# Performance work log

Hardware: AMD Instinct MI355X
Metric: run time of the kernel (lower is better)

## Reference

```python
import jax, jax.numpy as jnp
import numpy as np

N = 30000
IN_DIM = 256
OUT_DIM = 256
H = 4
HEAD_DIM = OUT_DIM // H  # 64
NUM_EDGE_TYPES = 20
NUM_USED_TYPES = 5  # len(EDGE_TYPES); global indices 0..4
E_PER_TYPE = 40000


def setup_inputs() -> dict:
    key = jax.random.key(0)
    ks = jax.random.split(key, 12)
    s = 0.05
    return {
        "h": jax.random.normal(ks[0], (N, IN_DIM), jnp.float32),
        "edge_src": jax.random.randint(ks[1], (NUM_USED_TYPES, E_PER_TYPE), 0, N, jnp.int64 if jax.config.jax_enable_x64 else jnp.int32),
        "edge_tgt": jax.random.randint(ks[2], (NUM_USED_TYPES, E_PER_TYPE), 0, N, jnp.int64 if jax.config.jax_enable_x64 else jnp.int32),
        "kqv_weight": jax.random.normal(ks[3], (3 * OUT_DIM, IN_DIM), jnp.float32) * s,
        "kqv_bias": jax.random.normal(ks[4], (3 * OUT_DIM,), jnp.float32) * s,
        "out_weight": jax.random.normal(ks[5], (OUT_DIM, OUT_DIM), jnp.float32) * s,
        "out_bias": jax.random.normal(ks[6], (OUT_DIM,), jnp.float32) * s,
        "k_rel": jax.random.normal(ks[7], (NUM_EDGE_TYPES, HEAD_DIM, HEAD_DIM), jnp.float32) * s,
        "v_rel": jax.random.normal(ks[8], (NUM_EDGE_TYPES, HEAD_DIM, HEAD_DIM), jnp.float32) * s,
        "skip": jax.random.normal(ks[9], (1,), jnp.float32),
        "p_rel": jax.random.normal(ks[10], (NUM_USED_TYPES, H), jnp.float32),
    }


def reference(h, edge_src, edge_tgt, kqv_weight, kqv_bias, out_weight, out_bias,
              k_rel, v_rel, skip, p_rel):
    n = h.shape[0]
    T, E = edge_src.shape
    d = HEAD_DIM

    # fused KQV projection: [N, 3*D]
    kqv = h @ kqv_weight.T + kqv_bias
    K, Q, V = jnp.split(kqv, 3, axis=-1)
    K = K.reshape(n, H, d)
    Q = Q.reshape(n, H, d)
    V = V.reshape(n, H, d)

    et = jnp.arange(T)  # global edge-type indices 0..T-1
    k_r = k_rel[et]     # [T, d, d]
    v_r = v_rel[et]

    # gather per-edge, per-type; apply relation matmuls
    K_rel = jnp.einsum('tehd,tdf->tehf', K[edge_src], k_r)  # [T,E,H,d]
    V_rel = jnp.einsum('tehd,tdf->tehf', V[edge_src], v_r)
    Q_tgt = Q[edge_tgt]                                     # [T,E,H,d]

    scale = float(d) ** (-0.5)
    alpha = (Q_tgt * K_rel).sum(-1) * scale                 # [T,E,H]
    alpha = alpha * p_rel[et][:, None, :]                   # multiplicative prior

    # flatten all edge types
    TE = T * E
    alpha = alpha.reshape(TE, H)
    V_rel = V_rel.reshape(TE, H, d)
    tgt_all = edge_tgt.reshape(TE)

    # segmented softmax over incoming edges per target node
    amax = jax.ops.segment_max(alpha, tgt_all, num_segments=n)       # [N,H]
    exp_alpha = jnp.exp(alpha - amax[tgt_all])
    exp_sum = jax.ops.segment_sum(exp_alpha, tgt_all, num_segments=n)
    attn = exp_alpha / (exp_sum[tgt_all] + 1e-16)                    # [TE,H]

    msg = attn[..., None] * V_rel                                    # [TE,H,d]
    out = jax.ops.segment_sum(msg, tgt_all, num_segments=n)          # [N,H,d]
    out = out.reshape(n, OUT_DIM)

    out = jax.nn.gelu(out, approximate=False)
    out = out @ out_weight.T + out_bias

    a = jax.nn.sigmoid(skip)  # [1], broadcasts
    return a * out + (1.0 - a) * h
```

## Files before the change

kernel.cpp:

```cpp
#include <hip/hip_runtime.h>
#include <hip/hip_bf16.h>
#include <math.h>

#define N_NODES 30000
#define NHEAD   4
#define HDIM    64
#define NTYPES  5
#define EPT     40000
#define TE      (NTYPES * EPT)
#define KDIM    256
#define NCAT    1792
#define NBLK    118

typedef __attribute__((ext_vector_type(8))) short short8;
typedef __attribute__((ext_vector_type(4))) float f32x4;

__device__ __forceinline__ unsigned short f2bf(float f) {
    __hip_bfloat16 h = __float2bfloat16(f);
    return *reinterpret_cast<unsigned short*>(&h);
}
__device__ __forceinline__ float bf2f(unsigned short u) {
    return __uint_as_float((unsigned)u << 16);
}

__device__ __forceinline__ void gload16(const unsigned short* g, unsigned short* l) {
    __builtin_amdgcn_global_load_lds((const __attribute__((address_space(1))) void*)g,
                                     (__attribute__((address_space(3))) void*)l, 16, 0, 0);
}

__global__ __launch_bounds__(256) void init_kernel(int* __restrict__ deg) {
    const int gid = blockIdx.x * blockDim.x + threadIdx.x;
    if (gid < N_NODES) deg[gid] = 0;
}

__global__ __launch_bounds__(256) void hist_kernel(const int* __restrict__ etgt,
                                                   int* __restrict__ deg) {
    const int stride = gridDim.x * blockDim.x;
    for (int i = blockIdx.x * blockDim.x + threadIdx.x; i < TE; i += stride)
        atomicAdd(&deg[etgt[i]], 1);
}

__global__ __launch_bounds__(256) void scan1_kernel(const int* __restrict__ deg,
                                                    int* __restrict__ bsum) {
    __shared__ int ws[4];
    const int t = threadIdx.x;
    const int gid = blockIdx.x * 256 + t;
    int d = (gid < N_NODES) ? deg[gid] : 0;
    d += __shfl_xor(d, 1);
    d += __shfl_xor(d, 2);
    d += __shfl_xor(d, 4);
    d += __shfl_xor(d, 8);
    d += __shfl_xor(d, 16);
    d += __shfl_xor(d, 32);
    if ((t & 63) == 0) ws[t >> 6] = d;
    __syncthreads();
    if (t == 0) bsum[blockIdx.x] = ws[0] + ws[1] + ws[2] + ws[3];
}

__global__ __launch_bounds__(128) void scan2_kernel(const int* __restrict__ bsum,
                                                    int* __restrict__ boff) {
    __shared__ int s[128];
    const int t = threadIdx.x;
    s[t] = (t < NBLK) ? bsum[t] : 0;
    __syncthreads();
    for (int d = 1; d < 128; d <<= 1) {
        const int v = (t >= d) ? s[t - d] : 0;
        __syncthreads();
        s[t] += v;
        __syncthreads();
    }
    if (t < NBLK) boff[t] = (t > 0) ? s[t - 1] : 0;
}

__global__ __launch_bounds__(256) void scan3_kernel(const int* __restrict__ deg,
                                                    const int* __restrict__ boff,
                                                    int* __restrict__ off,
                                                    int* __restrict__ cursor) {
    __shared__ int s[256];
    const int t = threadIdx.x;
    const int gid = blockIdx.x * 256 + t;
    const int d = (gid < N_NODES) ? deg[gid] : 0;
    s[t] = d;
    __syncthreads();
    for (int dd = 1; dd < 256; dd <<= 1) {
        const int v = (t >= dd) ? s[t - dd] : 0;
        __syncthreads();
        s[t] += v;
        __syncthreads();
    }
    if (gid < N_NODES) {
        const int excl = s[t] - d + boff[blockIdx.x];
        off[gid] = excl;
        cursor[gid] = excl;
    }
}

__global__ __launch_bounds__(256) void scatter_kernel(const int* __restrict__ etgt,
                                                      const int* __restrict__ esrc,
                                                      int* __restrict__ cursor,
                                                      int* __restrict__ perm) {
    const int stride = gridDim.x * blockDim.x;
    for (int e = blockIdx.x * blockDim.x + threadIdx.x; e < TE; e += stride) {
        const int pos = atomicAdd(&cursor[etgt[e]], 1);
        perm[pos] = esrc[e] | ((e / EPT) << 16);
    }
}

__global__ __launch_bounds__(256) void prep_all(const float* __restrict__ kqv_w,
                                                const float* __restrict__ kqv_b,
                                                const float* __restrict__ k_rel,
                                                const float* __restrict__ p_rel,
                                                const float* __restrict__ h,
                                                const float* __restrict__ v_rel,
                                                const float* __restrict__ out_w,
                                                unsigned short* __restrict__ Wcat,
                                                float* __restrict__ bias_cat,
                                                unsigned short* __restrict__ hb,
                                                unsigned short* __restrict__ vrelT,
                                                unsigned short* __restrict__ Wob) {
    const int bid = blockIdx.x;
    const int tid = threadIdx.x;
    if (bid < 1792) {
        const int r = bid, f = tid;
        if (r < 1280) {
            const int t = r >> 8, hh = (r >> 6) & 3, d = r & 63;
            const float sc = 0.125f * p_rel[t * NHEAD + hh];
            float acc = 0.f;
#pragma unroll
            for (int fp = 0; fp < 64; ++fp)
                acc = fmaf(kqv_w[(size_t)(hh * 64 + fp) * 256 + f], k_rel[t * 4096 + fp * 64 + d], acc);
            Wcat[(size_t)r * 256 + f] = f2bf(acc * sc);
            if (f == 0) {
                float b = 0.f;
#pragma unroll
                for (int fp = 0; fp < 64; ++fp)
                    b = fmaf(kqv_b[hh * 64 + fp], k_rel[t * 4096 + fp * 64 + d], b);
                bias_cat[r] = b * sc;
            }
        } else {
            const int src_row = r - 1024;
            Wcat[(size_t)r * 256 + f] = f2bf(kqv_w[(size_t)src_row * 256 + f]);
            if (f == 0) bias_cat[r] = kqv_b[src_row];
        }
    } else if (bid < 9292) {
        const int i = (bid - 1792) * 256 + tid;
        const float4 v = ((const float4*)h)[i];
        ushort4 u;
        u.x = f2bf(v.x); u.y = f2bf(v.y); u.z = f2bf(v.z); u.w = f2bf(v.w);
        ((ushort4*)hb)[i] = u;
    } else if (bid < 9372) {
        const int idx = (bid - 9292) * 256 + tid;
        if (idx < 64 * 320) {
            const int f = idx / 320, k = idx - f * 320;
            vrelT[f * 320 + k] = f2bf(v_rel[(k >> 6) * 4096 + (k & 63) * 64 + f]);
        }
    } else {
        const int i = (bid - 9372) * 256 + tid;
        Wob[i] = f2bf(out_w[i]);
    }
}

__global__ __launch_bounds__(256) void mfma_gemm(const unsigned short* __restrict__ hb,
                                                 const unsigned short* __restrict__ Wcat,
                                                 const float* __restrict__ bias_cat,
                                                 unsigned short* __restrict__ Ccat) {
    __shared__ unsigned short As[2][128 * 32];
    __shared__ unsigned short Bs[2][128 * 32];
    const int orig = blockIdx.x;
    const int xcd = orig & 7, pos = orig >> 3;
    const int q = 3290 / 8, r = 3290 % 8;
    const int wgid = (xcd < r ? xcd * (q + 1) : r * (q + 1) + (xcd - r) * q) + pos;
    const int brow0 = (wgid / 14) * 128;
    const int bcol0 = (wgid % 14) * 128;

    const int t = threadIdx.x;
    const int wid = t >> 6, lane = t & 63;
    const int wr = wid >> 1, wc = wid & 1;
    const int lrow = lane & 15, kb = lane >> 4;
    const int srow = lane >> 2;
    const int schunk = ((lane & 3) ^ ((lane >> 3) & 3)) * 8;
    const int rchunk = (kb ^ ((lrow >> 1) & 3)) * 8;

    const int arow0 = min(brow0 + wid * 16 + srow, N_NODES - 1);
    const int arow1 = min(brow0 + 64 + wid * 16 + srow, N_NODES - 1);
    const int brw0 = bcol0 + wid * 16 + srow;
    const int brw1 = bcol0 + 64 + wid * 16 + srow;

    auto stage = [&](int buf, int kt) {
        gload16(hb + (size_t)arow0 * KDIM + kt + schunk, &As[buf][wid * 512]);
        gload16(hb + (size_t)arow1 * KDIM + kt + schunk, &As[buf][2048 + wid * 512]);
        gload16(Wcat + (size_t)brw0 * KDIM + kt + schunk, &Bs[buf][wid * 512]);
        gload16(Wcat + (size_t)brw1 * KDIM + kt + schunk, &Bs[buf][2048 + wid * 512]);
    };

    f32x4 acc[4][4];
#pragma unroll
    for (int m = 0; m < 4; ++m)
#pragma unroll
        for (int n = 0; n < 4; ++n) acc[m][n] = (f32x4)0.f;

    stage(0, 0);
    __syncthreads();
    int cur = 0;
    for (int kt = 0; kt < KDIM; kt += 32) {
        if (kt + 32 < KDIM) stage(cur ^ 1, kt + 32);
        short8 af[4], bfr[4];
#pragma unroll
        for (int m = 0; m < 4; ++m)
            af[m] = *(const short8*)&As[cur][(wr * 64 + m * 16 + lrow) * 32 + rchunk];
#pragma unroll
        for (int n = 0; n < 4; ++n)
            bfr[n] = *(const short8*)&Bs[cur][(wc * 64 + n * 16 + lrow) * 32 + rchunk];
#pragma unroll
        for (int m = 0; m < 4; ++m)
#pragma unroll
            for (int n = 0; n < 4; ++n)
                acc[m][n] = __builtin_amdgcn_mfma_f32_16x16x32_bf16(af[m], bfr[n], acc[m][n], 0, 0, 0);
        __syncthreads();
        cur ^= 1;
    }

    unsigned short* Ts = &As[0][0];
    float bias4[4];
#pragma unroll
    for (int n = 0; n < 4; ++n) bias4[n] = bias_cat[bcol0 + wc * 64 + n * 16 + lrow];
    const int lrw = wr * 16 + kb * 4;
    const int lcw = wc * 64 + lrow;
#pragma unroll
    for (int m = 0; m < 4; ++m) {
        __syncthreads();
#pragma unroll
        for (int n = 0; n < 4; ++n)
#pragma unroll
            for (int v = 0; v < 4; ++v)
                Ts[(lrw + v) * 132 + lcw + n * 16] = f2bf(acc[m][n][v] + bias4[n]);
        __syncthreads();
#pragma unroll
        for (int rd = 0; rd < 2; ++rd) {
            const int lr = (t >> 4) + rd * 16;
            const int c0 = (t & 15) * 8;
            const int grow = brow0 + (lr >> 4) * 64 + m * 16 + (lr & 15);
            if (grow < N_NODES) {
                const uint2 lo = *(const uint2*)&Ts[lr * 132 + c0];
                const uint2 hi = *(const uint2*)&Ts[lr * 132 + c0 + 4];
                const uint4 o = make_uint4(lo.x, lo.y, hi.x, hi.y);
                *(uint4*)&Ccat[(size_t)grow * NCAT + bcol0 + c0] = o;
            }
        }
    }
}

__global__ __launch_bounds__(256) void edge_fused(const unsigned short* __restrict__ Ccat,
                                                  const int* __restrict__ off,
                                                  const int* __restrict__ perm,
                                                  unsigned short* __restrict__ Acat) {
    const int wid = threadIdx.x >> 6, lane = threadIdx.x & 63;
    const int tgt = (blockIdx.x << 2) + wid;
    const int h = lane >> 4, f0 = (lane & 15) << 2;
    const int off0 = off[tgt];
    const int off1 = (tgt == N_NODES - 1) ? TE : off[tgt + 1];
    const ushort4 qu = *(const ushort4*)(Ccat + (size_t)tgt * NCAT + 1280 + (h << 6) + f0);
    const float qx = bf2f(qu.x), qy = bf2f(qu.y), qz = bf2f(qu.z), qw = bf2f(qu.w);
    const int voff = 1536 + (h << 6) + f0;
    float es = 0.f;
    float4 a0 = make_float4(0, 0, 0, 0), a1 = a0, a2 = a0, a3 = a0, a4 = a0;
    int i = off0;
    while (i < off1) {
        const bool two = (i + 1 < off1);
        const int pk0 = perm[i];
        const int pk1 = two ? perm[i + 1] : pk0;
        const int s0 = pk0 & 0xFFFF, t0 = pk0 >> 16;
        const int s1 = pk1 & 0xFFFF, t1 = pk1 >> 16;
        const size_t rb0 = (size_t)s0 * NCAT, rb1 = (size_t)s1 * NCAT;
        const ushort4 ku0 = *(const ushort4*)(Ccat + rb0 + ((t0 * 4 + h) << 6) + f0);
        const ushort4 vu0 = *(const ushort4*)(Ccat + rb0 + voff);
        const ushort4 ku1 = *(const ushort4*)(Ccat + rb1 + ((t1 * 4 + h) << 6) + f0);
        const ushort4 vu1 = *(const ushort4*)(Ccat + rb1 + voff);
        float p0 = qx * bf2f(ku0.x) + qy * bf2f(ku0.y) + qz * bf2f(ku0.z) + qw * bf2f(ku0.w);
        float p1 = qx * bf2f(ku1.x) + qy * bf2f(ku1.y) + qz * bf2f(ku1.z) + qw * bf2f(ku1.w);
        p0 += __shfl_xor(p0, 1); p1 += __shfl_xor(p1, 1);
        p0 += __shfl_xor(p0, 2); p1 += __shfl_xor(p1, 2);
        p0 += __shfl_xor(p0, 4); p1 += __shfl_xor(p1, 4);
        p0 += __shfl_xor(p0, 8); p1 += __shfl_xor(p1, 8);
        {
            const float ex = __expf(p0);
            es += ex;
            const float mx = ex * bf2f(vu0.x), my = ex * bf2f(vu0.y);
            const float mz = ex * bf2f(vu0.z), mw = ex * bf2f(vu0.w);
            if (t0 == 0)      { a0.x += mx; a0.y += my; a0.z += mz; a0.w += mw; }
            else if (t0 == 1) { a1.x += mx; a1.y += my; a1.z += mz; a1.w += mw; }
            else if (t0 == 2) { a2.x += mx; a2.y += my; a2.z += mz; a2.w += mw; }
            else if (t0 == 3) { a3.x += mx; a3.y += my; a3.z += mz; a3.w += mw; }
            else              { a4.x += mx; a4.y += my; a4.z += mz; a4.w += mw; }
        }
        if (two) {
            const float ex = __expf(p1);
            es += ex;
            const float mx = ex * bf2f(vu1.x), my = ex * bf2f(vu1.y);
            const float mz = ex * bf2f(vu1.z), mw = ex * bf2f(vu1.w);
            if (t1 == 0)      { a0.x += mx; a0.y += my; a0.z += mz; a0.w += mw; }
            else if (t1 == 1) { a1.x += mx; a1.y += my; a1.z += mz; a1.w += mw; }
            else if (t1 == 2) { a2.x += mx; a2.y += my; a2.z += mz; a2.w += mw; }
            else if (t1 == 3) { a3.x += mx; a3.y += my; a3.z += mz; a3.w += mw; }
            else              { a4.x += mx; a4.y += my; a4.z += mz; a4.w += mw; }
        }
        i += two ? 2 : 1;
    }
    const float inv = 1.f / (es + 1e-16f);
    const size_t rr = (size_t)tgt * NHEAD + h;
    unsigned short* base = Acat + rr * (NTYPES * HDIM) + f0;
    ushort4 u;
    u.x = f2bf(a0.x * inv); u.y = f2bf(a0.y * inv); u.z = f2bf(a0.z * inv); u.w = f2bf(a0.w * inv);
    *(ushort4*)(base + 0 * HDIM) = u;
    u.x = f2bf(a1.x * inv); u.y = f2bf(a1.y * inv); u.z = f2bf(a1.z * inv); u.w = f2bf(a1.w * inv);
    *(ushort4*)(base + 1 * HDIM) = u;
    u.x = f2bf(a2.x * inv); u.y = f2bf(a2.y * inv); u.z = f2bf(a2.z * inv); u.w = f2bf(a2.w * inv);
    *(ushort4*)(base + 2 * HDIM) = u;
    u.x = f2bf(a3.x * inv); u.y = f2bf(a3.y * inv); u.z = f2bf(a3.z * inv); u.w = f2bf(a3.w * inv);
    *(ushort4*)(base + 3 * HDIM) = u;
    u.x = f2bf(a4.x * inv); u.y = f2bf(a4.y * inv); u.z = f2bf(a4.z * inv); u.w = f2bf(a4.w * inv);
    *(ushort4*)(base + 4 * HDIM) = u;
}

__global__ __launch_bounds__(256) void gemm_cat_mfma(const unsigned short* __restrict__ Acat,
                                                     const unsigned short* __restrict__ vrelT,
                                                     unsigned short* __restrict__ aggVb) {
    __shared__ unsigned short As[256 * 40];
    __shared__ unsigned short Bs[64 * 40];
    const int brow0 = blockIdx.x * 256;
    const int t = threadIdx.x;
    const int wid = t >> 6, lane = t & 63;
    const int lrow = lane & 15, kb = lane >> 4;
    const int r0 = t >> 2, q0 = (t & 3) * 8;

    f32x4 acc[4][4];
#pragma unroll
    for (int m = 0; m < 4; ++m)
#pragma unroll
        for (int n = 0; n < 4; ++n) acc[m][n] = (f32x4)0.f;

    for (int kt = 0; kt < 320; kt += 32) {
        uint4 a[4];
#pragma unroll
        for (int i = 0; i < 4; ++i) {
            const int row = min(brow0 + r0 + 64 * i, 120000 - 1);
            a[i] = *(const uint4*)(Acat + (size_t)row * 320 + kt + q0);
        }
        const uint4 b0 = *(const uint4*)(vrelT + (size_t)r0 * 320 + kt + q0);
        __syncthreads();
#pragma unroll
        for (int i = 0; i < 4; ++i)
            *(uint4*)&As[(r0 + 64 * i) * 40 + q0] = a[i];
        *(uint4*)&Bs[r0 * 40 + q0] = b0;
        __syncthreads();
        short8 af[4], bf_[4];
#pragma unroll
        for (int m = 0; m < 4; ++m)
            af[m] = *(const short8*)&As[(wid * 64 + m * 16 + lrow) * 40 + kb * 8];
#pragma unroll
        for (int n = 0; n < 4; ++n)
            bf_[n] = *(const short8*)&Bs[(n * 16 + lrow) * 40 + kb * 8];
#pragma unroll
        for (int m = 0; m < 4; ++m)
#pragma unroll
            for (int n = 0; n < 4; ++n)
                acc[m][n] = __builtin_amdgcn_mfma_f32_16x16x32_bf16(af[m], bf_[n], acc[m][n], 0, 0, 0);
    }

#pragma unroll
    for (int m = 0; m < 4; ++m) {
        const int gr0 = brow0 + wid * 64 + m * 16 + kb * 4;
#pragma unroll
        for (int v = 0; v < 4; ++v) {
            const int grow = gr0 + v;
            if (grow < 120000) {
#pragma unroll
                for (int n = 0; n < 4; ++n) {
                    const int gcol = n * 16 + lrow;
                    const float x = acc[m][n][v];
                    const float g = 0.5f * x * (1.f + erff(x * 0.7071067811865475f));
                    aggVb[(size_t)grow * 64 + gcol] = f2bf(g);
                }
            }
        }
    }
}

__global__ __launch_bounds__(256) void gemm_out_mfma(const unsigned short* __restrict__ A,
                                                     const unsigned short* __restrict__ Wob,
                                                     const float* __restrict__ bias,
                                                     float* __restrict__ C,
                                                     const unsigned short* __restrict__ hres,
                                                     const float* __restrict__ skip) {
    __shared__ unsigned short As[128 * 40];
    __shared__ unsigned short Bs[128 * 40];
    const int brow0 = blockIdx.x * 128;
    const int bcol0 = blockIdx.y * 128;
    const int t = threadIdx.x;
    const int wid = t >> 6, lane = t & 63;
    const int wr = wid >> 1, wc = wid & 1;
    const int lrow = lane & 15, kb = lane >> 4;
    const int r0 = t >> 2, q0 = t & 3;
    const int r1 = (t + 256) >> 2, q1 = t & 3;

    f32x4 acc[4][4];
#pragma unroll
    for (int m = 0; m < 4; ++m)
#pragma unroll
        for (int n = 0; n < 4; ++n) acc[m][n] = (f32x4)0.f;

    for (int kt = 0; kt < 256; kt += 32) {
        const int ar0 = min(brow0 + r0, N_NODES - 1);
        const int ar1 = min(brow0 + r1, N_NODES - 1);
        const uint4 a0 = *(const uint4*)(A + (size_t)ar0 * 256 + kt + q0 * 8);
        const uint4 a1 = *(const uint4*)(A + (size_t)ar1 * 256 + kt + q1 * 8);
        const uint4 b0 = *(const uint4*)(Wob + (size_t)(bcol0 + r0) * 256 + kt + q0 * 8);
        const uint4 b1 = *(const uint4*)(Wob + (size_t)(bcol0 + r1) * 256 + kt + q1 * 8);
        __syncthreads();
        *(uint4*)&As[r0 * 40 + q0 * 8] = a0;
        *(uint4*)&As[r1 * 40 + q1 * 8] = a1;
        *(uint4*)&Bs[r0 * 40 + q0 * 8] = b0;
        *(uint4*)&Bs[r1 * 40 + q1 * 8] = b1;
        __syncthreads();
        short8 af[4], bf_[4];
#pragma unroll
        for (int m = 0; m < 4; ++m)
            af[m] = *(const short8*)&As[(wr * 64 + m * 16 + lrow) * 40 + kb * 8];
#pragma unroll
        for (int n = 0; n < 4; ++n)
            bf_[n] = *(const short8*)&Bs[(wc * 64 + n * 16 + lrow) * 40 + kb * 8];
#pragma unroll
        for (int m = 0; m < 4; ++m)
#pragma unroll
            for (int n = 0; n < 4; ++n)
                acc[m][n] = __builtin_amdgcn_mfma_f32_16x16x32_bf16(af[m], bf_[n], acc[m][n], 0, 0, 0);
    }

    const float s = skip[0];
    const float sa = 1.f / (1.f + expf(-s));
    const float sb = 1.f - sa;
    float bias4[4];
#pragma unroll
    for (int n = 0; n < 4; ++n) bias4[n] = bias[bcol0 + wc * 64 + n * 16 + lrow];
#pragma unroll
    for (int m = 0; m < 4; ++m) {
        const int gr0 = brow0 + wr * 64 + m * 16 + kb * 4;
#pragma unroll
        for (int v = 0; v < 4; ++v) {
            const int grow = gr0 + v;
            if (grow < N_NODES) {
#pragma unroll
                for (int n = 0; n < 4; ++n) {
                    const int gcol = bcol0 + wc * 64 + n * 16 + lrow;
                    const float val = acc[m][n][v] + bias4[n];
                    C[(size_t)grow * 256 + gcol] = sa * val + sb * bf2f(hres[(size_t)grow * 256 + gcol]);
                }
            }
        }
    }
}

extern "C" void kernel_launch(void* const* d_in, const int* in_sizes, int n_in,
                              void* d_out, int out_size, void* d_ws, size_t ws_size,
                              hipStream_t stream) {
    const float* h      = (const float*)d_in[0];
    const int*   esrc   = (const int*)d_in[1];
    const int*   etgt   = (const int*)d_in[2];
    const float* kqv_w  = (const float*)d_in[3];
    const float* kqv_b  = (const float*)d_in[4];
    const float* out_w  = (const float*)d_in[5];
    const float* out_b  = (const float*)d_in[6];
    const float* k_rel  = (const float*)d_in[7];
    const float* v_rel  = (const float*)d_in[8];
    const float* skip   = (const float*)d_in[9];
    const float* p_rel  = (const float*)d_in[10];
    float* out = (float*)d_out;

    float* ws = (float*)d_ws;
    unsigned short* Ccat     = (unsigned short*)ws;
    int*            deg      = (int*)(ws + 26880000);
    int*            off      = (int*)(ws + 26910000);
    int*            cursor   = (int*)(ws + 26940000);
    int*            perm     = (int*)(ws + 26970000);
    unsigned short* aggVb    = (unsigned short*)(ws + 27170000);
    unsigned short* Acat     = (unsigned short*)(ws + 31010000);
    unsigned short* vrelT    = (unsigned short*)(ws + 50210000);
    unsigned short* Wob      = (unsigned short*)(ws + 50220240);
    unsigned short* hb       = (unsigned short*)(ws + 50253008);
    int*            bsum     = (int*)(ws + 54093008);
    int*            boff     = (int*)(ws + 54093126);
    unsigned short* Wcat     = (unsigned short*)(ws + 45370000);
    float*          bias_cat = ws + 45600000;

    hipLaunchKernelGGL(init_kernel, dim3(NBLK), dim3(256), 0, stream, deg);
    hipLaunchKernelGGL(hist_kernel, dim3(782), dim3(256), 0, stream, etgt, deg);
    hipLaunchKernelGGL(scan1_kernel, dim3(NBLK), dim3(256), 0, stream, deg, bsum);
    hipLaunchKernelGGL(scan2_kernel, dim3(1), dim3(128), 0, stream, bsum, boff);
    hipLaunchKernelGGL(scan3_kernel, dim3(NBLK), dim3(256), 0, stream, deg, boff, off, cursor);
    hipLaunchKernelGGL(scatter_kernel, dim3(782), dim3(256), 0, stream, etgt, esrc, cursor, perm);
    hipLaunchKernelGGL(prep_all, dim3(9628), dim3(256), 0, stream,
                       kqv_w, kqv_b, k_rel, p_rel, h, v_rel, out_w,
                       Wcat, bias_cat, hb, vrelT, Wob);
    hipLaunchKernelGGL(mfma_gemm, dim3(3290), dim3(256), 0, stream,
                       hb, Wcat, bias_cat, Ccat);
    hipLaunchKernelGGL(edge_fused, dim3(N_NODES / 4), dim3(256), 0, stream,
                       Ccat, off, perm, Acat);
    hipLaunchKernelGGL(gemm_cat_mfma, dim3(469), dim3(256), 0, stream,
                       Acat, vrelT, aggVb);
    hipLaunchKernelGGL(gemm_out_mfma, dim3(235, 2), dim3(256), 0, stream,
                       aggVb, Wob, out_b, out, hb, skip);
}
```

Baseline: 201.5 us.

## Fuse V-relation GEMM with GELU and output projection into one tail kernel

```diff
diff --git a/kernel.cpp b/kernel.cpp
--- a/kernel.cpp
+++ b/kernel.cpp
@@ -322,138 +322,134 @@
     *(ushort4*)(base + 4 * HDIM) = u;
 }
 
-__global__ __launch_bounds__(256) void gemm_cat_mfma(const unsigned short* __restrict__ Acat,
-                                                     const unsigned short* __restrict__ vrelT,
-                                                     unsigned short* __restrict__ aggVb) {
-    __shared__ unsigned short As[256 * 40];
-    __shared__ unsigned short Bs[64 * 40];
-    const int brow0 = blockIdx.x * 256;
+__global__ __launch_bounds__(512) void tail_fused(const unsigned short* __restrict__ Acat,
+                                                  const unsigned short* __restrict__ vrelT,
+                                                  const unsigned short* __restrict__ Wob,
+                                                  const float* __restrict__ bias,
+                                                  float* __restrict__ C,
+                                                  const unsigned short* __restrict__ hres,
+                                                  const float* __restrict__ skip) {
+    __shared__ unsigned short GsAs[128 * 264];
+    __shared__ unsigned short Pb[2][256 * 32];
     const int t = threadIdx.x;
     const int wid = t >> 6, lane = t & 63;
     const int lrow = lane & 15, kb = lane >> 4;
-    const int r0 = t >> 2, q0 = (t & 3) * 8;
-
-    f32x4 acc[4][4];
-#pragma unroll
-    for (int m = 0; m < 4; ++m)
-#pragma unroll
-        for (int n = 0; n < 4; ++n) acc[m][n] = (f32x4)0.f;
-
-    for (int kt = 0; kt < 320; kt += 32) {
-        uint4 a[4];
-#pragma unroll
-        for (int i = 0; i < 4; ++i) {
-            const int row = min(brow0 + r0 + 64 * i, 120000 - 1);
-            a[i] = *(const uint4*)(Acat + (size_t)row * 320 + kt + q0);
-        }
-        const uint4 b0 = *(const uint4*)(vrelT + (size_t)r0 * 320 + kt + q0);
-        __syncthreads();
-#pragma unroll
-        for (int i = 0; i < 4; ++i)
-            *(uint4*)&As[(r0 + 64 * i) * 40 + q0] = a[i];
-        *(uint4*)&Bs[r0 * 40 + q0] = b0;
-        __syncthreads();
-        short8 af[4], bf_[4];
+    const int n0 = blockIdx.x * 128;
+    const size_t ar0 = (size_t)n0 * 4;
+
+    {
+        unsigned short* As1 = GsAs;
+        unsigned short* Bs1 = &Pb[0][0];
+        const int r0 = t >> 2, q0 = (t & 3) * 8;
+        f32x4 acc[4][4];
 #pragma unroll
         for (int m = 0; m < 4; ++m)
-            af[m] = *(const short8*)&As[(wid * 64 + m * 16 + lrow) * 40 + kb * 8];
-#pragma unroll
-        for (int n = 0; n < 4; ++n)
-            bf_[n] = *(const short8*)&Bs[(n * 16 + lrow) * 40 + kb * 8];
+#pragma unroll
+            for (int n = 0; n < 4; ++n) acc[m][n] = (f32x4)0.f;
+
+        for (int kt = 0; kt < 320; kt += 32) {
+            uint4 a[4];
+#pragma unroll
+            for (int i = 0; i < 4; ++i) {
+                const size_t row = min(ar0 + r0 + 128 * i, (size_t)120000 - 1);
+                a[i] = *(const uint4*)(Acat + row * 320 + kt + q0);
+            }
+            uint4 b0;
+            if (t < 256) b0 = *(const uint4*)(vrelT + (size_t)r0 * 320 + kt + q0);
+            __syncthreads();
+#pragma unroll
+            for (int i = 0; i < 4; ++i)
+                *(uint4*)&As1[(r0 + 128 * i) * 40 + q0] = a[i];
+            if (t < 256) *(uint4*)&Bs1[r0 * 40 + q0] = b0;
+            __syncthreads();
+            short8 af[4], bf_[4];
+#pragma unroll
+            for (int m = 0; m < 4; ++m)
+                af[m] = *(const short8*)&As1[(wid * 64 + m * 16 + lrow) * 40 + kb * 8];
+#pragma unroll
+            for (int n = 0; n < 4; ++n)
+                bf_[n] = *(const short8*)&Bs1[(n * 16 + lrow) * 40 + kb * 8];
+#pragma unroll
+            for (int m = 0; m < 4; ++m)
+#pragma unroll
+                for (int n = 0; n < 4; ++n)
+                    acc[m][n] = __builtin_amdgcn_mfma_f32_16x16x32_bf16(af[m], bf_[n], acc[m][n], 0, 0, 0);
+            __syncthreads();
+        }
 #pragma unroll
         for (int m = 0; m < 4; ++m)
 #pragma unroll
-            for (int n = 0; n < 4; ++n)
-                acc[m][n] = __builtin_amdgcn_mfma_f32_16x16x32_bf16(af[m], bf_[n], acc[m][n], 0, 0, 0);
-    }
-
-#pragma unroll
-    for (int m = 0; m < 4; ++m) {
-        const int gr0 = brow0 + wid * 64 + m * 16 + kb * 4;
-#pragma unroll
-        for (int v = 0; v < 4; ++v) {
-            const int grow = gr0 + v;
-            if (grow < 120000) {
+            for (int v = 0; v < 4; ++v) {
+                const int lr = wid * 64 + m * 16 + kb * 4 + v;
 #pragma unroll
                 for (int n = 0; n < 4; ++n) {
-                    const int gcol = n * 16 + lrow;
+                    const int col = n * 16 + lrow;
                     const float x = acc[m][n][v];
                     const float g = 0.5f * x * (1.f + erff(x * 0.7071067811865475f));
-                    aggVb[(size_t)grow * 64 + gcol] = f2bf(g);
+                    GsAs[(lr >> 2) * 264 + (lr & 3) * 64 + col] = f2bf(g);
                 }
             }
-        }
-    }
-}
-
-__global__ __launch_bounds__(256) void gemm_out_mfma(const unsigned short* __restrict__ A,
-                                                     const unsigned short* __restrict__ Wob,
-                                                     const float* __restrict__ bias,
-                                                     float* __restrict__ C,
-                                                     const unsigned short* __restrict__ hres,
-                                                     const float* __restrict__ skip) {
-    __shared__ unsigned short As[128 * 40];
-    __shared__ unsigned short Bs[128 * 40];
-    const int brow0 = blockIdx.x * 128;
-    const int bcol0 = blockIdx.y * 128;
-    const int t = threadIdx.x;
-    const int wid = t >> 6, lane = t & 63;
-    const int wr = wid >> 1, wc = wid & 1;
-    const int lrow = lane & 15, kb = lane >> 4;
-    const int r0 = t >> 2, q0 = t & 3;
-    const int r1 = (t + 256) >> 2, q1 = t & 3;
-
-    f32x4 acc[4][4];
-#pragma unroll
-    for (int m = 0; m < 4; ++m)
-#pragma unroll
-        for (int n = 0; n < 4; ++n) acc[m][n] = (f32x4)0.f;
-
-    for (int kt = 0; kt < 256; kt += 32) {
-        const int ar0 = min(brow0 + r0, N_NODES - 1);
-        const int ar1 = min(brow0 + r1, N_NODES - 1);
-        const uint4 a0 = *(const uint4*)(A + (size_t)ar0 * 256 + kt + q0 * 8);
-        const uint4 a1 = *(const uint4*)(A + (size_t)ar1 * 256 + kt + q1 * 8);
-        const uint4 b0 = *(const uint4*)(Wob + (size_t)(bcol0 + r0) * 256 + kt + q0 * 8);
-        const uint4 b1 = *(const uint4*)(Wob + (size_t)(bcol0 + r1) * 256 + kt + q1 * 8);
-        __syncthreads();
-        *(uint4*)&As[r0 * 40 + q0 * 8] = a0;
-        *(uint4*)&As[r1 * 40 + q1 * 8] = a1;
-        *(uint4*)&Bs[r0 * 40 + q0 * 8] = b0;
-        *(uint4*)&Bs[r1 * 40 + q1 * 8] = b1;
-        __syncthreads();
-        short8 af[4], bf_[4];
+        __syncthreads();
+    }
+
+    {
+        const int wr = wid >> 2, wc = wid & 3;
+        const int rchunk = (kb ^ ((lrow >> 1) & 3)) * 8;
+        auto stage2 = [&](int buf, int kt) {
+#pragma unroll
+            for (int j = 0; j < 2; ++j) {
+                const int rowbase = (wid + 8 * j) * 16;
+                const int srow = rowbase + (lane >> 2);
+                const int gq = ((lane & 3) ^ ((lane >> 3) & 3)) * 8;
+                gload16(Wob + (size_t)srow * 256 + kt + gq, &Pb[buf][rowbase * 32]);
+            }
+        };
+        f32x4 acc[4][4];
 #pragma unroll
         for (int m = 0; m < 4; ++m)
-            af[m] = *(const short8*)&As[(wr * 64 + m * 16 + lrow) * 40 + kb * 8];
-#pragma unroll
-        for (int n = 0; n < 4; ++n)
-            bf_[n] = *(const short8*)&Bs[(wc * 64 + n * 16 + lrow) * 40 + kb * 8];
-#pragma unroll
-        for (int m = 0; m < 4; ++m)
+#pragma unroll
+            for (int n = 0; n < 4; ++n) acc[m][n] = (f32x4)0.f;
+
+        stage2(0, 0);
+        __syncthreads();
+        int cur = 0;
+        for (int kt = 0; kt < 256; kt += 32) {
+            if (kt + 32 < 256) stage2(cur ^ 1, kt + 32);
+            short8 af[4], bfr[4];
+#pragma unroll
+            for (int m = 0; m < 4; ++m)
+                af[m] = *(const short8*)&GsAs[(wr * 64 + m * 16 + lrow) * 264 + kt + kb * 8];
 #pragma unroll
             for (int n = 0; n < 4; ++n)
-                acc[m][n] = __builtin_amdgcn_mfma_f32_16x16x32_bf16(af[m], bf_[n], acc[m][n], 0, 0, 0);
-    }
-
-    const float s = skip[0];
-    const float sa = 1.f / (1.f + expf(-s));
-    const float sb = 1.f - sa;
-    float bias4[4];
-#pragma unroll
-    for (int n = 0; n < 4; ++n) bias4[n] = bias[bcol0 + wc * 64 + n * 16 + lrow];
-#pragma unroll
-    for (int m = 0; m < 4; ++m) {
-        const int gr0 = brow0 + wr * 64 + m * 16 + kb * 4;
-#pragma unroll
-        for (int v = 0; v < 4; ++v) {
-            const int grow = gr0 + v;
-            if (grow < N_NODES) {
-#pragma unroll
-                for (int n = 0; n < 4; ++n) {
-                    const int gcol = bcol0 + wc * 64 + n * 16 + lrow;
-                    const float val = acc[m][n][v] + bias4[n];
-                    C[(size_t)grow * 256 + gcol] = sa * val + sb * bf2f(hres[(size_t)grow * 256 + gcol]);
+                bfr[n] = *(const short8*)&Pb[cur][(wc * 64 + n * 16 + lrow) * 32 + rchunk];
+#pragma unroll
+            for (int m = 0; m < 4; ++m)
+#pragma unroll
+                for (int n = 0; n < 4; ++n)
+                    acc[m][n] = __builtin_amdgcn_mfma_f32_16x16x32_bf16(af[m], bfr[n], acc[m][n], 0, 0, 0);
+            __syncthreads();
+            cur ^= 1;
+        }
+
+        const float s = skip[0];
+        const float sa = 1.f / (1.f + expf(-s));
+        const float sb = 1.f - sa;
+        float bias4[4];
+#pragma unroll
+        for (int n = 0; n < 4; ++n) bias4[n] = bias[wc * 64 + n * 16 + lrow];
+#pragma unroll
+        for (int m = 0; m < 4; ++m) {
+            const int gr0 = n0 + wr * 64 + m * 16 + kb * 4;
+#pragma unroll
+            for (int v = 0; v < 4; ++v) {
+                const int grow = gr0 + v;
+                if (grow < N_NODES) {
+#pragma unroll
+                    for (int n = 0; n < 4; ++n) {
+                        const int gcol = wc * 64 + n * 16 + lrow;
+                        const float val = acc[m][n][v] + bias4[n];
+                        C[(size_t)grow * 256 + gcol] = sa * val + sb * bf2f(hres[(size_t)grow * 256 + gcol]);
+                    }
                 }
             }
         }
@@ -482,7 +478,6 @@
     int*            off      = (int*)(ws + 26910000);
     int*            cursor   = (int*)(ws + 26940000);
     int*            perm     = (int*)(ws + 26970000);
-    unsigned short* aggVb    = (unsigned short*)(ws + 27170000);
     unsigned short* Acat     = (unsigned short*)(ws + 31010000);
     unsigned short* vrelT    = (unsigned short*)(ws + 50210000);
     unsigned short* Wob      = (unsigned short*)(ws + 50220240);
@@ -505,8 +500,6 @@
                        hb, Wcat, bias_cat, Ccat);
     hipLaunchKernelGGL(edge_fused, dim3(N_NODES / 4), dim3(256), 0, stream,
                        Ccat, off, perm, Acat);
-    hipLaunchKernelGGL(gemm_cat_mfma, dim3(469), dim3(256), 0, stream,
-                       Acat, vrelT, aggVb);
-    hipLaunchKernelGGL(gemm_out_mfma, dim3(235, 2), dim3(256), 0, stream,
-                       aggVb, Wob, out_b, out, hb, skip);
-}
+    hipLaunchKernelGGL(tail_fused, dim3(235), dim3(512), 0, stream,
+                       Acat, vrelT, Wob, out_b, out, hb, skip);
+}
```

Measured after the change: 198.6 us. About the same (-1.4%).
